# Optimization experiments

Hardware: AMD Instinct MI355X
Metric: run time of the kernel (lower is better)

The kernel has to match this reference:

```python
import jax, jax.numpy as jnp
import numpy as np

CHUNK = 128
KERNEL_EPS = 1e-4
ATTN_EPS = 1e-6


def _gaussian_orthogonal_random_matrix(nb_rows, nb_cols, seed=0):
    # scaling=0: rows of stacked orthogonal blocks, scaled by chi-distributed norms
    rng = np.random.default_rng(seed)
    blocks = []
    n_full = nb_rows // nb_cols
    for _ in range(n_full):
        qm, _ = np.linalg.qr(rng.standard_normal((nb_cols, nb_cols)))
        blocks.append(qm.T)
    rem = nb_rows - n_full * nb_cols
    if rem > 0:
        qm, _ = np.linalg.qr(rng.standard_normal((nb_cols, nb_cols)))
        blocks.append(qm.T[:rem])
    mat = np.concatenate(blocks, axis=0)
    multiplier = np.linalg.norm(rng.standard_normal((nb_rows, nb_cols)), axis=1)
    return (multiplier[:, None] * mat).astype(np.float32)


def softmax_kernel(data, proj, is_query):
    # data: [b,h,n,d], proj: [m,d]
    d = data.shape[-1]
    m = proj.shape[0]
    data_normalizer = d ** -0.25
    ratio = m ** -0.5
    data_dash = jnp.einsum('bhnd,md->bhnm', data * data_normalizer, proj)
    diag_data = (data ** 2).sum(-1, keepdims=True) * 0.5 * (data_normalizer ** 2)
    if is_query:
        stab = jnp.max(data_dash, axis=-1, keepdims=True)
    else:
        stab = jnp.max(data_dash)
    return ratio * (jnp.exp(data_dash - diag_data - stab) + KERNEL_EPS)


def chunked_causal_linear_attention(qf, kf, v):
    # qf,kf: [b,h,n,m]; v: [b,h,n,e]
    b, h, n, m = qf.shape
    e = v.shape[-1]
    nc = n // CHUNK
    to_chunks = lambda t: t.reshape(b, h, nc, CHUNK, -1).transpose(2, 0, 1, 3, 4)
    qc, kc, vc = to_chunks(qf), to_chunks(kf), to_chunks(v)  # [nc,b,h,c,*]

    def step(carry, xs):
        Z, S = carry  # Z: [b,h,m], S: [b,h,m,e]
        q, k, vv = xs
        k_cum = Z[:, :, None, :] + jnp.cumsum(k, axis=2)          # [b,h,c,m]
        D_inv = 1.0 / jnp.einsum('bhcm,bhcm->bhc', q, k_cum + ATTN_EPS)
        ctx = jnp.einsum('bhcm,bhce->bhcme', k, vv)               # [b,h,c,m,e]
        ctx_cum = S[:, :, None, :, :] + jnp.cumsum(ctx, axis=2)
        out = jnp.einsum('bhcme,bhcm,bhc->bhce', ctx_cum, q, D_inv)
        return (k_cum[:, :, -1, :], ctx_cum[:, :, -1, :, :]), out

    Z0 = jnp.zeros((b, h, m), qf.dtype)
    S0 = jnp.zeros((b, h, m, e), qf.dtype)
    (Z, S), outs = jax.lax.scan(jax.checkpoint(step), (Z0, S0), (qc, kc, vc))
    out = outs.transpose(1, 2, 0, 3, 4).reshape(b, h, n, e)
    return out, Z, S


def setup_inputs() -> dict:
    key = jax.random.key(0)
    kq, kk, kv = jax.random.split(key, 3)
    B, H, N, D, M = 2, 8, 4096, 64, 256
    q = jax.random.normal(kq, (B, H, N, D), dtype=jnp.float32)
    k = jax.random.normal(kk, (B, H, N, D), dtype=jnp.float32)
    v = jax.random.normal(kv, (B, H, N, D), dtype=jnp.float32)
    projection_matrix = jnp.asarray(_gaussian_orthogonal_random_matrix(M, D))
    return {"q": q, "k": k, "v": v, "projection_matrix": projection_matrix,
            "inferrring_states": 1}


def reference(q, k, v, projection_matrix, inferrring_states):
    qf = softmax_kernel(q, projection_matrix, is_query=True)
    kf = softmax_kernel(k, projection_matrix, is_query=False)
    out, Z, S = chunked_causal_linear_attention(qf, kf, v)
    return (out, Z, S)
```

## Files before the change

### kernel.cpp

```cpp
#include <hip/hip_runtime.h>

typedef unsigned short ushort_t;
typedef __attribute__((ext_vector_type(8))) short bf16x8;
typedef __attribute__((ext_vector_type(8))) _Float16 f16x8;
typedef __attribute__((ext_vector_type(16))) float f32x16;

#define NORMC 0.35355339059327373f
#define DIAGC 0.0625f
#define RATIO 0.0625f
#define KEPS  1e-4f
#define AEPS  1e-6f
#define KAPPA (RATIO*KEPS)

__device__ __forceinline__ unsigned short f2bf(float f){
  unsigned u = __float_as_uint(f);
  unsigned r = (u + 0x7FFFu + ((u >> 16) & 1u)) >> 16;
  return (unsigned short)r;
}
__device__ __forceinline__ float bf2f(unsigned short h){
  return __uint_as_float(((unsigned)h) << 16);
}
__device__ __forceinline__ unsigned enc_f(float f){
  unsigned u = __float_as_uint(f);
  return (u & 0x80000000u) ? ~u : (u | 0x80000000u);
}
__device__ __forceinline__ float dec_f(unsigned e){
  unsigned b = (e & 0x80000000u) ? (e ^ 0x80000000u) : ~e;
  return __uint_as_float(b);
}
__device__ __forceinline__ unsigned short h2u(_Float16 h){
  union { _Float16 h; unsigned short u; } c; c.h = h; return c.u;
}
__device__ __forceinline__ unsigned pk2h(float a, float b){
  return (unsigned)h2u((_Float16)a) | ((unsigned)h2u((_Float16)b) << 16);
}
__device__ __forceinline__ unsigned cvt2(unsigned wrd, float alpha){
  float lo = bf2f((ushort_t)(wrd & 0xffffu));
  float hi = bf2f((ushort_t)(wrd >> 16));
  return (unsigned)f2bf(fmaf(alpha, lo, KAPPA)) |
         ((unsigned)f2bf(fmaf(alpha, hi, KAPPA)) << 16);
}

__global__ void k_prep(const float* __restrict__ proj, ushort_t* __restrict__ pjh,
                       unsigned* __restrict__ kmax){
  int t = threadIdx.x;
  if (t == 0) *kmax = 0u;
  for (int d = 0; d < 64; ++d){
    float val = NORMC * proj[t*64 + d];
    pjh[t*64 + d] = h2u((_Float16)val);
  }
}

__launch_bounds__(512, 2)
__global__ void k_chunkF(const float* __restrict__ kk, const float* __restrict__ v,
                         const ushort_t* __restrict__ pjh,
                         ushort_t* __restrict__ kfp, float* __restrict__ Zl,
                         float* __restrict__ Sl, float* __restrict__ vsb,
                         unsigned* __restrict__ kmax, float* __restrict__ lmArr)
{
  extern __shared__ char sm[];
  char* Bp = sm;
  char* Xh = sm + 32768;
  char* Xl = sm + 49152;
  char* ob = sm;
  char* kT = sm + 65536;
  char* vT = sm + 131072;
  float* dsm  = (float*)(sm + 147456);
  float* wred = (float*)(sm + 147968);

  int tid = threadIdx.x;
  int w   = tid >> 6;
  int wr  = w & 3;
  int wc  = w >> 2;
  int lane= tid & 63;
  int l31 = lane & 31;
  int half= lane >> 5;
  int cb  = (int)blockIdx.x;
  int bh  = cb >> 5, j = cb & 31;
  int row0 = bh*4096 + j*128;

  for (int i = tid; i < 2048; i += 512){
    int m = i >> 3, c8 = i & 7;
    int rgn = ((m>>5)*4 + (c8>>1))*2 + (c8&1);
    int slot = (m & 31) ^ ((rgn & 7) << 2);
    *(uint4*)(Bp + rgn*512 + slot*16) = *(const uint4*)(pjh + m*64 + c8*8);
  }
  #pragma unroll
  for (int it = 0; it < 4; ++it){
    int g = it*512 + tid;
    int row = g >> 4, c4 = g & 15;
    float4 xv = *(const float4*)(kk + (size_t)(row0+row)*64 + c4*4);
    _Float16 h0=(_Float16)xv.x, h1=(_Float16)xv.y, h2=(_Float16)xv.z, h3=(_Float16)xv.w;
    float l0 = xv.x-(float)h0, l1 = xv.y-(float)h1, l2 = xv.z-(float)h2, l3 = xv.w-(float)h3;
    int rgn = ((row>>5)*4 + (c4>>2))*2 + ((c4>>1)&1);
    int off = rgn*512 + (((row&31) ^ ((c4>>1)<<2)))*16 + (c4&1)*8;
    uint2 ph; ph.x = (unsigned)h2u(h0)|((unsigned)h2u(h1)<<16);
              ph.y = (unsigned)h2u(h2)|((unsigned)h2u(h3)<<16);
    uint2 pl; pl.x = pk2h(l0,l1); pl.y = pk2h(l2,l3);
    *(uint2*)(Xh + off) = ph;
    *(uint2*)(Xl + off) = pl;
    float ssq = xv.x*xv.x + xv.y*xv.y + xv.z*xv.z + xv.w*xv.w;
    ssq += __shfl_xor(ssq, 1); ssq += __shfl_xor(ssq, 2);
    ssq += __shfl_xor(ssq, 4); ssq += __shfl_xor(ssq, 8);
    if ((tid & 15) == 0) dsm[row] = ssq;
  }
  {
    int e = tid & 63, c0 = tid >> 6;
    int swz = (e & 15) << 4;
    #pragma unroll
    for (int u=0; u<16; ++u){
      int c = c0 + u*8;
      *(ushort_t*)(vT + e*256 + ((c*2) ^ swz)) = f2bf(v[(size_t)(row0+c)*64 + e]);
    }
  }
  __syncthreads();

  f16x8 ah[4], al[4];
  #pragma unroll
  for (int ks = 0; ks < 4; ++ks){
    int rgn = (wr*4+ks)*2+half;
    int off = rgn*512 + ((l31 ^ ((2*ks+half)<<2)))*16;
    ah[ks] = *(const f16x8*)(Xh + off);
    al[ks] = *(const f16x8*)(Xl + off);
  }
  f32x16 acc[4];
  #pragma unroll
  for (int ct=0; ct<4; ++ct){
    #pragma unroll
    for (int r=0; r<16; ++r) acc[ct][r] = 0.f;
  }
  #pragma unroll
  for (int ks = 0; ks < 4; ++ks){
    #pragma unroll
    for (int ct=0; ct<4; ++ct){
      int ctg = wc*4 + ct;
      int rgn = (ctg*4+ks)*2+half;
      f16x8 bv = *(const f16x8*)(Bp + rgn*512 + ((l31 ^ ((2*ks+half)<<2)))*16);
      acc[ct] = __builtin_amdgcn_mfma_f32_32x32x16_f16(ah[ks], bv, acc[ct], 0, 0, 0);
      acc[ct] = __builtin_amdgcn_mfma_f32_32x32x16_f16(al[ks], bv, acc[ct], 0, 0, 0);
    }
  }

  {
    float wm = acc[0][0];
    #pragma unroll
    for (int ct=0; ct<4; ++ct){
      #pragma unroll
      for (int r=0; r<16; ++r) wm = fmaxf(wm, acc[ct][r]);
    }
    #pragma unroll
    for (int s=1; s<32; s<<=1) wm = fmaxf(wm, __shfl_xor(wm, s));
    wm = fmaxf(wm, __shfl_xor(wm, 32));
    if (lane == 0) wred[w] = wm;
  }
  __syncthreads();
  float lmb = wred[0];
  #pragma unroll
  for (int i=1;i<8;++i) lmb = fmaxf(lmb, wred[i]);
  if (tid == 0){
    lmArr[cb] = lmb;
    atomicMax(kmax, enc_f(lmb));
  }
  float dgv[16];
  #pragma unroll
  for (int r=0; r<16; ++r)
    dgv[r] = DIAGC * dsm[32*wr + (r&3) + 8*(r>>2) + 4*half];

  #pragma unroll
  for (int ct=0; ct<4; ++ct){
    int m = wc*128 + ct*32 + l31;
    int swm = (m & 15) << 4;
    #pragma unroll
    for (int g=0; g<4; ++g){
      unsigned pk0=0, pk1=0;
      #pragma unroll
      for (int rr=0; rr<4; ++rr){
        int r = g*4 + rr;
        int c = 32*wr + rr + 8*g + 4*half;
        float e = __expf(acc[ct][r] - dgv[r] - lmb);
        unsigned b = f2bf(e);
        if (rr < 2) pk0 |= b << (16*rr); else pk1 |= b << (16*(rr-2));
        *(ushort_t*)(ob + c*512 + ((m*2) ^ ((c&15)<<4))) = (ushort_t)b;
      }
      int c0 = 32*wr + 8*g + 4*half;
      *(uint2*)(kT + m*256 + ((c0*2) ^ swm)) = make_uint2(pk0, pk1);
    }
  }
  __syncthreads();

  f32x16 acc2[2], accz, avs[2];
  #pragma unroll
  for (int et=0;et<2;++et){
    #pragma unroll
    for (int r=0;r<16;++r){ acc2[et][r]=0.f; avs[et][r]=0.f; }
  }
  #pragma unroll
  for (int r=0;r<16;++r) accz[r]=0.f;
  bf16x8 onesB, onesA;
  #pragma unroll
  for (int i=0;i<8;++i){
    onesB[i] = (l31==0) ? (short)0x3F80 : (short)0;
    onesA[i] = (short)0x3F80;
  }
  int mrow = 32*w + l31;
  int swm2 = (mrow & 15) << 4;
  #pragma unroll
  for (int ks=0; ks<8; ++ks){
    int koff = ks*32 + half*16;
    bf16x8 af = *(const bf16x8*)(kT + mrow*256 + (koff ^ swm2));
    bf16x8 b0 = *(const bf16x8*)(vT + (l31)*256      + (koff ^ ((l31&15)<<4)));
    bf16x8 b1 = *(const bf16x8*)(vT + (32+l31)*256   + (koff ^ (((32+l31)&15)<<4)));
    acc2[0] = __builtin_amdgcn_mfma_f32_32x32x16_bf16(af, b0, acc2[0], 0, 0, 0);
    acc2[1] = __builtin_amdgcn_mfma_f32_32x32x16_bf16(af, b1, acc2[1], 0, 0, 0);
    accz    = __builtin_amdgcn_mfma_f32_32x32x16_bf16(af, onesB, accz, 0, 0, 0);
    if (w == 0){
      avs[0] = __builtin_amdgcn_mfma_f32_32x32x16_bf16(onesA, b0, avs[0], 0, 0, 0);
      avs[1] = __builtin_amdgcn_mfma_f32_32x32x16_bf16(onesA, b1, avs[1], 0, 0, 0);
    }
  }
  #pragma unroll
  for (int r=0; r<16; ++r){
    int m = 32*w + (r&3) + 8*(r>>2) + 4*half;
    #pragma unroll
    for (int et=0; et<2; ++et)
      Sl[(size_t)cb*16384 + (size_t)m*64 + et*32 + l31] = acc2[et][r];
  }
  if (l31 == 0){
    #pragma unroll
    for (int r=0; r<16; ++r){
      int m = 32*w + (r&3) + 8*(r>>2) + 4*half;
      Zl[(size_t)cb*256 + m] = accz[r];
    }
  }
  if (w == 0 && half == 0){
    vsb[(size_t)cb*64 + l31]      = avs[0][0];
    vsb[(size_t)cb*64 + 32 + l31] = avs[1][0];
  }
  {
    ushort_t* dst = kfp + (size_t)row0*256;
    for (int i = tid; i < 4096; i += 512){
      int row = i >> 5, s = i & 31;
      uint4 d = *(const uint4*)(ob + row*512 + ((s*16) ^ ((row&15)<<4)));
      *(uint4*)(dst + (size_t)row*256 + ((s ^ (row&15)))*8) = d;
    }
  }
}

__launch_bounds__(256)
__global__ void k_scan(float* __restrict__ Zl, const float* __restrict__ Sl,
                       const float* __restrict__ vsb, const float* __restrict__ lmArr,
                       const unsigned* __restrict__ kmax,
                       ushort_t* __restrict__ S0b,
                       float* __restrict__ outZ, float* __restrict__ outS){
  float gm = dec_f(*kmax);
  int t = threadIdx.x;
  int bh = blockIdx.x / 65;
  int s  = blockIdx.x % 65;
  if (s == 64){
    size_t base = (size_t)(bh*32)*256 + t;
    float rz = 0.f;
    #pragma unroll
    for (int j0=0;j0<32;j0+=8){
      float x[8];
      #pragma unroll
      for (int u=0;u<8;++u){
        int cbx = bh*32 + j0 + u;
        float a = RATIO * __expf(lmArr[cbx] - gm);
        x[u] = fmaf(a, Zl[base + (size_t)(j0+u)*256], KAPPA*128.f);
      }
      #pragma unroll
      for (int u=0;u<8;++u){ Zl[base + (size_t)(j0+u)*256] = rz; rz += x[u]; }
    }
    outZ[(size_t)bh*256 + t] = rz;
  } else {
    int e = t & 63;
    size_t base = (size_t)(bh*32)*16384 + (size_t)s*256 + t;
    float rs = 0.f;
    #pragma unroll
    for (int j0=0;j0<32;j0+=8){
      float x[8];
      #pragma unroll
      for (int u=0;u<8;++u){
        int cbx = bh*32 + j0 + u;
        float a = RATIO * __expf(lmArr[cbx] - gm);
        x[u] = fmaf(a, Sl[base + (size_t)(j0+u)*16384], KAPPA * vsb[(size_t)cbx*64 + e]);
      }
      #pragma unroll
      for (int u=0;u<8;++u){
        S0b[(size_t)(bh*32 + j0+u)*16384 + (size_t)s*256 + t] = f2bf(rs);
        rs += x[u];
      }
    }
    outS[(size_t)bh*16384 + (size_t)s*256 + t] = rs;
  }
}

__launch_bounds__(512, 2)
__global__ void k_outF(const float* __restrict__ q, const ushort_t* __restrict__ pjh,
                       const ushort_t* __restrict__ kfp, const float* __restrict__ v,
                       const ushort_t* __restrict__ S0b, const float* __restrict__ Zp,
                       const float* __restrict__ lmArr, const unsigned* __restrict__ kmax,
                       float* __restrict__ outO)
{
  extern __shared__ char sm[];
  char* Bp  = sm;
  char* Ab  = sm;
  char* qfb = sm + 32768;
  char* Xh  = sm + 32768;
  char* Xl  = sm + 49152;
  char* ktb = sm + 98304;
  char* s0t = sm + 114688;
  char* vTb = sm + 98304;
  float* dsm = (float*)(sm + 122880);
  float* rmx = (float*)(sm + 123392);
  float* qzc = (float*)(sm + 124416);
  float* rsc = (float*)(sm + 125440);
  float* rsf = (float*)(sm + 126464);

  int tid = threadIdx.x;
  int w   = tid >> 6;
  int wr  = w & 3;
  int wc  = w >> 2;
  int lane= tid & 63;
  int l31 = lane & 31;
  int half= lane >> 5;
  int pb  = (int)blockIdx.x;
  int bh  = pb >> 5, j = pb & 31;
  int row0 = bh*4096 + j*128;
  size_t qbase = (size_t)row0*256;

  float gmv = dec_f(*kmax);
  float alpha = RATIO * __expf(lmArr[pb] - gmv);

  for (int i = tid; i < 2048; i += 512){
    int m = i >> 3, c8 = i & 7;
    int rgn = ((m>>5)*4 + (c8>>1))*2 + (c8&1);
    int slot = (m & 31) ^ ((rgn & 7) << 2);
    *(uint4*)(Bp + rgn*512 + slot*16) = *(const uint4*)(pjh + m*64 + c8*8);
  }
  #pragma unroll
  for (int it = 0; it < 4; ++it){
    int g = it*512 + tid;
    int row = g >> 4, c4 = g & 15;
    float4 xv = *(const float4*)(q + (size_t)(row0+row)*64 + c4*4);
    _Float16 h0=(_Float16)xv.x, h1=(_Float16)xv.y, h2=(_Float16)xv.z, h3=(_Float16)xv.w;
    float l0 = xv.x-(float)h0, l1 = xv.y-(float)h1, l2 = xv.z-(float)h2, l3 = xv.w-(float)h3;
    int rgn = ((row>>5)*4 + (c4>>2))*2 + ((c4>>1)&1);
    int off = rgn*512 + (((row&31) ^ ((c4>>1)<<2)))*16 + (c4&1)*8;
    uint2 ph; ph.x = (unsigned)h2u(h0)|((unsigned)h2u(h1)<<16);
              ph.y = (unsigned)h2u(h2)|((unsigned)h2u(h3)<<16);
    uint2 pl; pl.x = pk2h(l0,l1); pl.y = pk2h(l2,l3);
    *(uint2*)(Xh + off) = ph;
    *(uint2*)(Xl + off) = pl;
    float ssq = xv.x*xv.x + xv.y*xv.y + xv.z*xv.z + xv.w*xv.w;
    ssq += __shfl_xor(ssq, 1); ssq += __shfl_xor(ssq, 2);
    ssq += __shfl_xor(ssq, 4); ssq += __shfl_xor(ssq, 8);
    if ((tid & 15) == 0) dsm[row] = ssq;
  }
  __syncthreads();

  f16x8 ah[4], al[4];
  #pragma unroll
  for (int ks = 0; ks < 4; ++ks){
    int rgn = (wr*4+ks)*2+half;
    int off = rgn*512 + ((l31 ^ ((2*ks+half)<<2)))*16;
    ah[ks] = *(const f16x8*)(Xh + off);
    al[ks] = *(const f16x8*)(Xl + off);
  }
  f32x16 acc[4];
  #pragma unroll
  for (int ct=0; ct<4; ++ct){
    #pragma unroll
    for (int r=0; r<16; ++r) acc[ct][r] = 0.f;
  }
  #pragma unroll
  for (int ks = 0; ks < 4; ++ks){
    #pragma unroll
    for (int ct=0; ct<4; ++ct){
      int ctg = wc*4 + ct;
      int rgn = (ctg*4+ks)*2+half;
      f16x8 bv = *(const f16x8*)(Bp + rgn*512 + ((l31 ^ ((2*ks+half)<<2)))*16);
      acc[ct] = __builtin_amdgcn_mfma_f32_32x32x16_f16(ah[ks], bv, acc[ct], 0, 0, 0);
      acc[ct] = __builtin_amdgcn_mfma_f32_32x32x16_f16(al[ks], bv, acc[ct], 0, 0, 0);
    }
  }
  {
    float rmax[16];
    #pragma unroll
    for (int r=0; r<16; ++r){
      float mx = acc[0][r];
      #pragma unroll
      for (int ct=1; ct<4; ++ct) mx = fmaxf(mx, acc[ct][r]);
      #pragma unroll
      for (int s=1; s<32; s<<=1) mx = fmaxf(mx, __shfl_xor(mx, s));
      rmax[r] = mx;
    }
    if (l31 == 0){
      #pragma unroll
      for (int r=0; r<16; ++r)
        rmx[wc*128 + 32*wr + (r&3) + 8*(r>>2) + 4*half] = rmax[r];
    }
  }
  __syncthreads();

  float qzp[16];
  #pragma unroll
  for (int r=0;r<16;++r) qzp[r] = 0.f;
  {
    float dgv[16], stv[16];
    #pragma unroll
    for (int r=0; r<16; ++r){
      int lrow = 32*wr + (r&3) + 8*(r>>2) + 4*half;
      dgv[r] = DIAGC * dsm[lrow];
      stv[r] = fmaxf(rmx[lrow], rmx[128+lrow]);
    }
    #pragma unroll
    for (int ct=0; ct<4; ++ct){
      int m = wc*128 + ct*32 + l31;
      float z0v = Zp[(size_t)pb*256 + m] + AEPS;
      #pragma unroll
      for (int r=0; r<16; ++r){
        int c = 32*wr + (r&3) + 8*(r>>2) + 4*half;
        float e = __expf(acc[ct][r] - dgv[r] - stv[r]);
        unsigned b = f2bf(RATIO*(e + KEPS));
        *(ushort_t*)(qfb + c*512 + ((m*2) ^ ((c&15)<<4))) = (ushort_t)b;
        qzp[r] += bf2f((ushort_t)b) * z0v;
      }
    }
    #pragma unroll
    for (int s=1; s<32; s<<=1){
      #pragma unroll
      for (int r=0;r<16;++r) qzp[r] += __shfl_xor(qzp[r], s);
    }
    if (l31 == 0){
      #pragma unroll
      for (int r=0;r<16;++r)
        qzc[wc*128 + 32*wr + (r&3) + 8*(r>>2) + 4*half] = qzp[r];
    }
  }

  f32x16 accA[2], acc2;
  #pragma unroll
  for (int ct2=0;ct2<2;++ct2){
    #pragma unroll
    for (int r=0;r<16;++r) accA[ct2][r] = 0.f;
  }
  #pragma unroll
  for (int r=0;r<16;++r) acc2[r] = 0.f;

  int arow = 32*wr + l31;
  for (int mt=0; mt<4; ++mt){
    int m0 = mt*64;
    __syncthreads();
    #pragma unroll
    for (int u=0;u<2;++u){
      int ci = tid*2+u; int rr = ci>>3, c8 = ci&7;
      int sw = (c8*16) ^ ((rr&7)<<4);
      uint4 rk = *(const uint4*)(kfp + qbase + (size_t)rr*256 + m0 + c8*8);
      uint4 ck; ck.x = cvt2(rk.x, alpha); ck.y = cvt2(rk.y, alpha);
                ck.z = cvt2(rk.z, alpha); ck.w = cvt2(rk.w, alpha);
      *(uint4*)(ktb + rr*128 + sw) = ck;
    }
    {
      int mm = tid >> 3, c8 = tid & 7;
      uint4 sv = *(const uint4*)(S0b + (size_t)pb*16384 + (size_t)(m0+mm)*64 + c8*8);
      unsigned wds[4] = {sv.x, sv.y, sv.z, sv.w};
      #pragma unroll
      for (int jj=0;jj<4;++jj){
        int e0 = c8*8 + jj*2, e1 = e0 + 1;
        int sw0 = ((e0&7) ^ ((e0>>3)&7)) << 4;
        int sw1 = ((e1&7) ^ ((e1>>3)&7)) << 4;
        *(ushort_t*)(s0t + e0*128 + ((mm*2) ^ sw0)) = (ushort_t)(wds[jj] & 0xffffu);
        *(ushort_t*)(s0t + e1*128 + ((mm*2) ^ sw1)) = (ushort_t)(wds[jj] >> 16);
      }
    }
    __syncthreads();
    #pragma unroll
    for (int ks=0;ks<4;++ks){
      bf16x8 af = *(const bf16x8*)(qfb + arow*512 + ((m0*2 + ks*32 + half*16) ^ ((arow&15)<<4)));
      {
        int er = wc*32 + l31;
        int sw = ((er&7) ^ ((er>>3)&7)) << 4;
        bf16x8 bS = *(const bf16x8*)(s0t + er*128 + ((ks*32 + half*16) ^ sw));
        acc2 = __builtin_amdgcn_mfma_f32_32x32x16_bf16(af, bS, acc2, 0, 0, 0);
      }
      #pragma unroll
      for (int ct2=0;ct2<2;++ct2){
        int c = wc*2 + ct2;
        if (c <= wr){
          int br = c*32 + l31;
          bf16x8 bfv = *(const bf16x8*)(ktb + br*128 + ((ks*32 + half*16) ^ ((br&7)<<4)));
          accA[ct2] = __builtin_amdgcn_mfma_f32_32x32x16_bf16(af, bfv, accA[ct2], 0, 0, 0);
        }
      }
    }
  }

  {
    float p[16];
    #pragma unroll
    for (int r=0;r<16;++r) p[r]=0.f;
    #pragma unroll
    for (int ct2=0;ct2<2;++ct2){
      int c = wc*2 + ct2;
      if (c <= wr){
        #pragma unroll
        for (int r=0;r<16;++r){
          int grow = 32*wr + (r&3) + 8*(r>>2) + 4*half;
          int col  = c*32 + l31;
          float mval = (col <= grow) ? accA[ct2][r] : 0.f;
          p[r] += mval;
          *(ushort_t*)(Ab + grow*256 + ((col*2) ^ ((grow&15)<<4))) = f2bf(mval);
        }
      }
    }
    #pragma unroll
    for (int s=1;s<32;s<<=1){
      #pragma unroll
      for (int r=0;r<16;++r) p[r] += __shfl_xor(p[r], s);
    }
    if (l31 == 0){
      #pragma unroll
      for (int r=0;r<16;++r)
        rsc[wc*128 + 32*wr + (r&3) + 8*(r>>2) + 4*half] = p[r];
    }
  }
  __syncthreads();

  {
    int e = tid & 63, c0 = tid >> 6;
    int swz = (e & 15) << 4;
    #pragma unroll
    for (int u=0; u<16; ++u){
      int c = c0 + u*8;
      *(ushort_t*)(vTb + e*256 + ((c*2) ^ swz)) = f2bf(v[(size_t)(row0+c)*64 + e]);
    }
  }
  __syncthreads();

  #pragma unroll
  for (int ks=0; ks<8; ++ks){
    if (ks <= 2*wr + 1){
      bf16x8 af = *(const bf16x8*)(Ab + arow*256 + ((ks*32 + half*16) ^ ((arow&15)<<4)));
      int er = wc*32 + l31;
      bf16x8 bfv = *(const bf16x8*)(vTb + er*256 + ((ks*32 + half*16) ^ ((er&15)<<4)));
      acc2 = __builtin_amdgcn_mfma_f32_32x32x16_bf16(af, bfv, acc2, 0, 0, 0);
    }
  }
  __syncthreads();
  if (tid < 128)
    rsf[tid] = 1.0f / (rsc[tid] + rsc[128+tid] + qzc[tid] + qzc[128+tid]);
  __syncthreads();
  #pragma unroll
  for (int r=0;r<16;++r){
    int grow = 32*wr + (r&3) + 8*(r>>2) + 4*half;
    int e = wc*32 + l31;
    outO[(size_t)(row0+grow)*64 + e] = acc2[r] * rsf[grow];
  }
}

extern "C" void kernel_launch(void* const* d_in, const int* in_sizes, int n_in,
                              void* d_out, int out_size, void* d_ws, size_t ws_size,
                              hipStream_t stream){
  (void)in_sizes; (void)n_in; (void)out_size; (void)ws_size;
  const float* q    = (const float*)d_in[0];
  const float* k    = (const float*)d_in[1];
  const float* v    = (const float*)d_in[2];
  const float* proj = (const float*)d_in[3];

  char* ws = (char*)d_ws;
  unsigned* kmax = (unsigned*)ws;
  float*    lmA  = (float*)(ws + 256);
  ushort_t* pjh  = (ushort_t*)(ws + 4096);
  ushort_t* kfp  = (ushort_t*)(ws + 65792);
  float*    Zl   = (float*)(ws + 65792 + 33554432);
  float*    Sl   = (float*)(ws + 65792 + 33554432 + 524288);
  ushort_t* S0b  = (ushort_t*)(ws + 65792 + 67633152);
  float*    vsb  = (float*)(ws + 65792 + 67633152 + 16777216);

  float* outO = (float*)d_out;
  float* outZ = outO + (size_t)2*8*4096*64;
  float* outS = outZ + 2*8*256;

  hipFuncSetAttribute((const void*)k_chunkF, hipFuncAttributeMaxDynamicSharedMemorySize, 148480);
  hipFuncSetAttribute((const void*)k_outF,   hipFuncAttributeMaxDynamicSharedMemorySize, 126976);

  k_prep  <<<1,     256, 0, stream>>>(proj, pjh, kmax);
  k_chunkF<<<512,   512, 148480, stream>>>(k, v, pjh, kfp, Zl, Sl, vsb, kmax, lmA);
  k_scan  <<<16*65, 256, 0, stream>>>(Zl, Sl, vsb, lmA, kmax, S0b, outZ, outS);
  k_outF  <<<512,   512, 126976, stream>>>(q, pjh, kfp, v, S0b, Zl, lmA, kmax, outO);
}
```

Measured before the change: 98.24 us.

## Transpose S layout, fold alpha/kappa rescale into MFMA epilogue, shrink outF LDS

The chunk kernel now produces per-chunk S transposed (e-major), so the output kernel can copy S0 and raw kf tiles straight into LDS with 16-byte stores. This removes the scalar scatter and the per-element alpha/kappa conversion. The alpha scaling and the kappa term are applied to the masked intra-chunk scores, and q·Z0 plus the row sums of qf are computed with an extra MFMA against a Z/ones vector. Query features are staged in 64-column slices, which cuts LDS from about 124KB to 75KB and may allow higher occupancy. A small new transpose kernel restores the m-major final S output, at the cost of an extra launch and extra MFMA work.

Result: slower. 147.3 us (+49.9%).

```diff
diff --git a/kernel.cpp b/kernel.cpp
--- a/kernel.cpp
+++ b/kernel.cpp
@@ -33,12 +33,6 @@
 }
 __device__ __forceinline__ unsigned pk2h(float a, float b){
   return (unsigned)h2u((_Float16)a) | ((unsigned)h2u((_Float16)b) << 16);
-}
-__device__ __forceinline__ unsigned cvt2(unsigned wrd, float alpha){
-  float lo = bf2f((ushort_t)(wrd & 0xffffu));
-  float hi = bf2f((ushort_t)(wrd >> 16));
-  return (unsigned)f2bf(fmaf(alpha, lo, KAPPA)) |
-         ((unsigned)f2bf(fmaf(alpha, hi, KAPPA)) << 16);
 }
 
 __global__ void k_prep(const float* __restrict__ proj, ushort_t* __restrict__ pjh,
@@ -188,11 +182,11 @@
   }
   __syncthreads();
 
-  f32x16 acc2[2], accz, avs[2];
+  f32x16 accS[2], accz, avs[2];
   #pragma unroll
   for (int et=0;et<2;++et){
     #pragma unroll
-    for (int r=0;r<16;++r){ acc2[et][r]=0.f; avs[et][r]=0.f; }
+    for (int r=0;r<16;++r){ accS[et][r]=0.f; avs[et][r]=0.f; }
   }
   #pragma unroll
   for (int r=0;r<16;++r) accz[r]=0.f;
@@ -202,28 +196,31 @@
     onesB[i] = (l31==0) ? (short)0x3F80 : (short)0;
     onesA[i] = (short)0x3F80;
   }
+  int erow = (w&1)*32 + l31;
+  int mc0  = ((w>>1)*2 + 0)*32 + l31;
+  int mc1  = ((w>>1)*2 + 1)*32 + l31;
   int mrow = 32*w + l31;
-  int swm2 = (mrow & 15) << 4;
   #pragma unroll
   for (int ks=0; ks<8; ++ks){
     int koff = ks*32 + half*16;
-    bf16x8 af = *(const bf16x8*)(kT + mrow*256 + (koff ^ swm2));
-    bf16x8 b0 = *(const bf16x8*)(vT + (l31)*256      + (koff ^ ((l31&15)<<4)));
-    bf16x8 b1 = *(const bf16x8*)(vT + (32+l31)*256   + (koff ^ (((32+l31)&15)<<4)));
-    acc2[0] = __builtin_amdgcn_mfma_f32_32x32x16_bf16(af, b0, acc2[0], 0, 0, 0);
-    acc2[1] = __builtin_amdgcn_mfma_f32_32x32x16_bf16(af, b1, acc2[1], 0, 0, 0);
-    accz    = __builtin_amdgcn_mfma_f32_32x32x16_bf16(af, onesB, accz, 0, 0, 0);
+    bf16x8 afv = *(const bf16x8*)(vT + erow*256 + (koff ^ ((erow&15)<<4)));
+    bf16x8 bk0 = *(const bf16x8*)(kT + mc0*256 + (koff ^ ((mc0&15)<<4)));
+    bf16x8 bk1 = *(const bf16x8*)(kT + mc1*256 + (koff ^ ((mc1&15)<<4)));
+    bf16x8 afk = *(const bf16x8*)(kT + mrow*256 + (koff ^ ((mrow&15)<<4)));
+    accS[0] = __builtin_amdgcn_mfma_f32_32x32x16_bf16(afv, bk0, accS[0], 0, 0, 0);
+    accS[1] = __builtin_amdgcn_mfma_f32_32x32x16_bf16(afv, bk1, accS[1], 0, 0, 0);
+    accz    = __builtin_amdgcn_mfma_f32_32x32x16_bf16(afk, onesB, accz, 0, 0, 0);
     if (w == 0){
-      avs[0] = __builtin_amdgcn_mfma_f32_32x32x16_bf16(onesA, b0, avs[0], 0, 0, 0);
-      avs[1] = __builtin_amdgcn_mfma_f32_32x32x16_bf16(onesA, b1, avs[1], 0, 0, 0);
+      bf16x8 bv1 = *(const bf16x8*)(vT + (32+l31)*256 + (koff ^ (((32+l31)&15)<<4)));
+      avs[0] = __builtin_amdgcn_mfma_f32_32x32x16_bf16(onesA, afv, avs[0], 0, 0, 0);
+      avs[1] = __builtin_amdgcn_mfma_f32_32x32x16_bf16(onesA, bv1, avs[1], 0, 0, 0);
     }
   }
   #pragma unroll
   for (int r=0; r<16; ++r){
-    int m = 32*w + (r&3) + 8*(r>>2) + 4*half;
-    #pragma unroll
-    for (int et=0; et<2; ++et)
-      Sl[(size_t)cb*16384 + (size_t)m*64 + et*32 + l31] = acc2[et][r];
+    int e = (w&1)*32 + (r&3) + 8*(r>>2) + 4*half;
+    Sl[(size_t)cb*16384 + (size_t)e*256 + ((w>>1)*2+0)*32 + l31] = accS[0][r];
+    Sl[(size_t)cb*16384 + (size_t)e*256 + ((w>>1)*2+1)*32 + l31] = accS[1][r];
   }
   if (l31 == 0){
     #pragma unroll
@@ -251,7 +248,7 @@
                        const float* __restrict__ vsb, const float* __restrict__ lmArr,
                        const unsigned* __restrict__ kmax,
                        ushort_t* __restrict__ S0b,
-                       float* __restrict__ outZ, float* __restrict__ outS){
+                       float* __restrict__ outZ, float* __restrict__ outSt){
   float gm = dec_f(*kmax);
   int t = threadIdx.x;
   int bh = blockIdx.x / 65;
@@ -273,7 +270,6 @@
     }
     outZ[(size_t)bh*256 + t] = rz;
   } else {
-    int e = t & 63;
     size_t base = (size_t)(bh*32)*16384 + (size_t)s*256 + t;
     float rs = 0.f;
     #pragma unroll
@@ -283,7 +279,7 @@
       for (int u=0;u<8;++u){
         int cbx = bh*32 + j0 + u;
         float a = RATIO * __expf(lmArr[cbx] - gm);
-        x[u] = fmaf(a, Sl[base + (size_t)(j0+u)*16384], KAPPA * vsb[(size_t)cbx*64 + e]);
+        x[u] = fmaf(a, Sl[base + (size_t)(j0+u)*16384], KAPPA * vsb[(size_t)cbx*64 + s]);
       }
       #pragma unroll
       for (int u=0;u<8;++u){
@@ -291,7 +287,24 @@
         rs += x[u];
       }
     }
-    outS[(size_t)bh*16384 + (size_t)s*256 + t] = rs;
+    outSt[(size_t)bh*16384 + (size_t)s*256 + t] = rs;
+  }
+}
+
+__launch_bounds__(256)
+__global__ void k_tr(const float* __restrict__ outSt, float* __restrict__ outS){
+  __shared__ float tl[64][65];
+  int tid = threadIdx.x;
+  int bh = blockIdx.x >> 2, mt = blockIdx.x & 3;
+  int m0 = mt*64;
+  for (int i = tid; i < 4096; i += 256){
+    int e = i >> 6, m = i & 63;
+    tl[e][m] = outSt[(size_t)bh*16384 + (size_t)e*256 + m0 + m];
+  }
+  __syncthreads();
+  for (int i = tid; i < 4096; i += 256){
+    int m = i >> 6, e = i & 63;
+    outS[(size_t)bh*16384 + (size_t)(m0+m)*64 + e] = tl[e][m];
   }
 }
 
@@ -303,19 +316,18 @@
                        float* __restrict__ outO)
 {
   extern __shared__ char sm[];
-  char* Bp  = sm;
-  char* Ab  = sm;
-  char* qfb = sm + 32768;
-  char* Xh  = sm + 32768;
-  char* Xl  = sm + 49152;
-  char* ktb = sm + 98304;
-  char* s0t = sm + 114688;
-  char* vTb = sm + 98304;
-  float* dsm = (float*)(sm + 122880);
-  float* rmx = (float*)(sm + 123392);
-  float* qzc = (float*)(sm + 124416);
-  float* rsc = (float*)(sm + 125440);
-  float* rsf = (float*)(sm + 126464);
+  char* Bp   = sm;
+  char* Ab   = sm;
+  char* Xh   = sm + 32768;
+  char* qft  = sm + 32768;
+  char* vTb  = sm + 32768;
+  char* Xl   = sm + 49152;
+  char* ktb  = sm + 49152;
+  char* s0t  = sm + 65536;
+  float* dsm = (float*)(sm + 73728);
+  float* rmx = (float*)(sm + 74240);
+  float* rsc = (float*)(sm + 75264);
+  ushort_t* z0b = (ushort_t*)(sm + 76288);
 
   int tid = threadIdx.x;
   int w   = tid >> 6;
@@ -357,6 +369,7 @@
     ssq += __shfl_xor(ssq, 4); ssq += __shfl_xor(ssq, 8);
     if ((tid & 15) == 0) dsm[row] = ssq;
   }
+  if (tid < 256) z0b[tid] = f2bf(Zp[(size_t)pb*256 + tid] + AEPS);
   __syncthreads();
 
   f16x8 ah[4], al[4];
@@ -403,50 +416,29 @@
   }
   __syncthreads();
 
-  float qzp[16];
-  #pragma unroll
-  for (int r=0;r<16;++r) qzp[r] = 0.f;
-  {
-    float dgv[16], stv[16];
-    #pragma unroll
-    for (int r=0; r<16; ++r){
-      int lrow = 32*wr + (r&3) + 8*(r>>2) + 4*half;
-      dgv[r] = DIAGC * dsm[lrow];
-      stv[r] = fmaxf(rmx[lrow], rmx[128+lrow]);
-    }
-    #pragma unroll
-    for (int ct=0; ct<4; ++ct){
-      int m = wc*128 + ct*32 + l31;
-      float z0v = Zp[(size_t)pb*256 + m] + AEPS;
-      #pragma unroll
-      for (int r=0; r<16; ++r){
-        int c = 32*wr + (r&3) + 8*(r>>2) + 4*half;
-        float e = __expf(acc[ct][r] - dgv[r] - stv[r]);
-        unsigned b = f2bf(RATIO*(e + KEPS));
-        *(ushort_t*)(qfb + c*512 + ((m*2) ^ ((c&15)<<4))) = (ushort_t)b;
-        qzp[r] += bf2f((ushort_t)b) * z0v;
-      }
-    }
-    #pragma unroll
-    for (int s=1; s<32; s<<=1){
-      #pragma unroll
-      for (int r=0;r<16;++r) qzp[r] += __shfl_xor(qzp[r], s);
-    }
-    if (l31 == 0){
-      #pragma unroll
-      for (int r=0;r<16;++r)
-        qzc[wc*128 + 32*wr + (r&3) + 8*(r>>2) + 4*half] = qzp[r];
-    }
-  }
-
-  f32x16 accA[2], acc2;
+  unsigned qpk[2][16];
+  #pragma unroll
+  for (int r=0; r<16; ++r){
+    int lrow = 32*wr + (r&3) + 8*(r>>2) + 4*half;
+    float dg = DIAGC * dsm[lrow];
+    float st = fmaxf(rmx[lrow], rmx[128+lrow]);
+    #pragma unroll
+    for (int p=0; p<2; ++p){
+      float e0 = __expf(acc[2*p][r]   - dg - st);
+      float e1 = __expf(acc[2*p+1][r] - dg - st);
+      qpk[p][r] = (unsigned)f2bf(RATIO*(e0+KEPS)) |
+                  ((unsigned)f2bf(RATIO*(e1+KEPS)) << 16);
+    }
+  }
+
+  f32x16 accA[2], acc2, accQ;
   #pragma unroll
   for (int ct2=0;ct2<2;++ct2){
     #pragma unroll
     for (int r=0;r<16;++r) accA[ct2][r] = 0.f;
   }
   #pragma unroll
-  for (int r=0;r<16;++r) acc2[r] = 0.f;
+  for (int r=0;r<16;++r){ acc2[r] = 0.f; accQ[r] = 0.f; }
 
   int arow = 32*wr + l31;
   for (int mt=0; mt<4; ++mt){
@@ -455,45 +447,60 @@
     #pragma unroll
     for (int u=0;u<2;++u){
       int ci = tid*2+u; int rr = ci>>3, c8 = ci&7;
-      int sw = (c8*16) ^ ((rr&7)<<4);
-      uint4 rk = *(const uint4*)(kfp + qbase + (size_t)rr*256 + m0 + c8*8);
-      uint4 ck; ck.x = cvt2(rk.x, alpha); ck.y = cvt2(rk.y, alpha);
-                ck.z = cvt2(rk.z, alpha); ck.w = cvt2(rk.w, alpha);
-      *(uint4*)(ktb + rr*128 + sw) = ck;
+      *(uint4*)(ktb + rr*128 + ((c8*16) ^ ((rr&7)<<4))) =
+          *(const uint4*)(kfp + qbase + (size_t)rr*256 + m0 + c8*8);
     }
     {
-      int mm = tid >> 3, c8 = tid & 7;
-      uint4 sv = *(const uint4*)(S0b + (size_t)pb*16384 + (size_t)(m0+mm)*64 + c8*8);
-      unsigned wds[4] = {sv.x, sv.y, sv.z, sv.w};
-      #pragma unroll
-      for (int jj=0;jj<4;++jj){
-        int e0 = c8*8 + jj*2, e1 = e0 + 1;
-        int sw0 = ((e0&7) ^ ((e0>>3)&7)) << 4;
-        int sw1 = ((e1&7) ^ ((e1>>3)&7)) << 4;
-        *(ushort_t*)(s0t + e0*128 + ((mm*2) ^ sw0)) = (ushort_t)(wds[jj] & 0xffffu);
-        *(ushort_t*)(s0t + e1*128 + ((mm*2) ^ sw1)) = (ushort_t)(wds[jj] >> 16);
+      int e = tid >> 3, c8 = tid & 7;
+      *(uint4*)(s0t + e*128 + ((c8*16) ^ ((e&7)<<4))) =
+          *(const uint4*)(S0b + (size_t)pb*16384 + (size_t)e*256 + m0 + c8*8);
+    }
+    if (wc == (mt>>1)){
+      int p = mt & 1;
+      #pragma unroll
+      for (int r=0;r<16;++r){
+        int c = 32*wr + (r&3) + 8*(r>>2) + 4*half;
+        int sw = (c&7)<<4;
+        *(ushort_t*)(qft + c*128 + ((l31*2) ^ sw))      = (ushort_t)(qpk[p][r] & 0xffffu);
+        *(ushort_t*)(qft + c*128 + (((32+l31)*2) ^ sw)) = (ushort_t)(qpk[p][r] >> 16);
       }
     }
     __syncthreads();
     #pragma unroll
     for (int ks=0;ks<4;++ks){
-      bf16x8 af = *(const bf16x8*)(qfb + arow*512 + ((m0*2 + ks*32 + half*16) ^ ((arow&15)<<4)));
+      int ko = ks*32 + half*16;
+      bf16x8 af = *(const bf16x8*)(qft + arow*128 + (ko ^ ((arow&7)<<4)));
       {
         int er = wc*32 + l31;
-        int sw = ((er&7) ^ ((er>>3)&7)) << 4;
-        bf16x8 bS = *(const bf16x8*)(s0t + er*128 + ((ks*32 + half*16) ^ sw));
+        bf16x8 bS = *(const bf16x8*)(s0t + er*128 + (ko ^ ((er&7)<<4)));
         acc2 = __builtin_amdgcn_mfma_f32_32x32x16_bf16(af, bS, acc2, 0, 0, 0);
+      }
+      {
+        bf16x8 zb = {};
+        if (l31 == 0) zb = *(const bf16x8*)((const char*)z0b + m0*2 + ko);
+        if (l31 == 1){
+          #pragma unroll
+          for (int i2=0;i2<8;++i2) zb[i2] = (short)0x3F80;
+        }
+        accQ = __builtin_amdgcn_mfma_f32_32x32x16_bf16(af, zb, accQ, 0, 0, 0);
       }
       #pragma unroll
       for (int ct2=0;ct2<2;++ct2){
         int c = wc*2 + ct2;
         if (c <= wr){
           int br = c*32 + l31;
-          bf16x8 bfv = *(const bf16x8*)(ktb + br*128 + ((ks*32 + half*16) ^ ((br&7)<<4)));
-          accA[ct2] = __builtin_amdgcn_mfma_f32_32x32x16_bf16(af, bfv, accA[ct2], 0, 0, 0);
+          bf16x8 bk = *(const bf16x8*)(ktb + br*128 + (ko ^ ((br&7)<<4)));
+          accA[ct2] = __builtin_amdgcn_mfma_f32_32x32x16_bf16(af, bk, accA[ct2], 0, 0, 0);
         }
       }
     }
+  }
+
+  float qzv[16], qfsv[16];
+  #pragma unroll
+  for (int r=0;r<16;++r){
+    qzv[r]  = __shfl(accQ[r], half*32 + 0);
+    qfsv[r] = __shfl(accQ[r], half*32 + 1);
   }
 
   {
@@ -508,16 +515,16 @@
         for (int r=0;r<16;++r){
           int grow = 32*wr + (r&3) + 8*(r>>2) + 4*half;
           int col  = c*32 + l31;
-          float mval = (col <= grow) ? accA[ct2][r] : 0.f;
+          float mval = (col <= grow) ? fmaf(alpha, accA[ct2][r], KAPPA*qfsv[r]) : 0.f;
           p[r] += mval;
           *(ushort_t*)(Ab + grow*256 + ((col*2) ^ ((grow&15)<<4))) = f2bf(mval);
         }
       }
     }
     #pragma unroll
-    for (int s=1;s<32;s<<=1){
-      #pragma unroll
-      for (int r=0;r<16;++r) p[r] += __shfl_xor(p[r], s);
+    for (int s2=1;s2<32;s2<<=1){
+      #pragma unroll
+      for (int r=0;r<16;++r) p[r] += __shfl_xor(p[r], s2);
     }
     if (l31 == 0){
       #pragma unroll
@@ -543,19 +550,16 @@
     if (ks <= 2*wr + 1){
       bf16x8 af = *(const bf16x8*)(Ab + arow*256 + ((ks*32 + half*16) ^ ((arow&15)<<4)));
       int er = wc*32 + l31;
-      bf16x8 bfv = *(const bf16x8*)(vTb + er*256 + ((ks*32 + half*16) ^ ((er&15)<<4)));
-      acc2 = __builtin_amdgcn_mfma_f32_32x32x16_bf16(af, bfv, acc2, 0, 0, 0);
-    }
-  }
-  __syncthreads();
-  if (tid < 128)
-    rsf[tid] = 1.0f / (rsc[tid] + rsc[128+tid] + qzc[tid] + qzc[128+tid]);
-  __syncthreads();
+      bf16x8 bv = *(const bf16x8*)(vTb + er*256 + ((ks*32 + half*16) ^ ((er&15)<<4)));
+      acc2 = __builtin_amdgcn_mfma_f32_32x32x16_bf16(af, bv, acc2, 0, 0, 0);
+    }
+  }
+
   #pragma unroll
   for (int r=0;r<16;++r){
     int grow = 32*wr + (r&3) + 8*(r>>2) + 4*half;
-    int e = wc*32 + l31;
-    outO[(size_t)(row0+grow)*64 + e] = acc2[r] * rsf[grow];
+    float dv = 1.0f / (rsc[grow] + rsc[128+grow] + qzv[r]);
+    outO[(size_t)(row0+grow)*64 + wc*32 + l31] = acc2[r] * dv;
   }
 }
 
@@ -573,20 +577,22 @@
   float*    lmA  = (float*)(ws + 256);
   ushort_t* pjh  = (ushort_t*)(ws + 4096);
   ushort_t* kfp  = (ushort_t*)(ws + 65792);
-  float*    Zl   = (float*)(ws + 65792 + 33554432);
-  float*    Sl   = (float*)(ws + 65792 + 33554432 + 524288);
-  ushort_t* S0b  = (ushort_t*)(ws + 65792 + 67633152);
-  float*    vsb  = (float*)(ws + 65792 + 67633152 + 16777216);
+  float*    Zl   = (float*)(ws + 33620224);
+  float*    Sl   = (float*)(ws + 34144512);
+  ushort_t* S0b  = (ushort_t*)(ws + 67698944);
+  float*    vsb  = (float*)(ws + 84476160);
+  float*    oSt  = (float*)(ws + 84607232);
 
   float* outO = (float*)d_out;
   float* outZ = outO + (size_t)2*8*4096*64;
   float* outS = outZ + 2*8*256;
 
   hipFuncSetAttribute((const void*)k_chunkF, hipFuncAttributeMaxDynamicSharedMemorySize, 148480);
-  hipFuncSetAttribute((const void*)k_outF,   hipFuncAttributeMaxDynamicSharedMemorySize, 126976);
+  hipFuncSetAttribute((const void*)k_outF,   hipFuncAttributeMaxDynamicSharedMemorySize, 76800);
 
   k_prep  <<<1,     256, 0, stream>>>(proj, pjh, kmax);
   k_chunkF<<<512,   512, 148480, stream>>>(k, v, pjh, kfp, Zl, Sl, vsb, kmax, lmA);
-  k_scan  <<<16*65, 256, 0, stream>>>(Zl, Sl, vsb, lmA, kmax, S0b, outZ, outS);
-  k_outF  <<<512,   512, 126976, stream>>>(q, pjh, kfp, v, S0b, Zl, lmA, kmax, outO);
-}
+  k_scan  <<<16*65, 256, 0, stream>>>(Zl, Sl, vsb, lmA, kmax, S0b, outZ, oSt);
+  k_tr    <<<64,    256, 0, stream>>>(oSt, outS);
+  k_outF  <<<512,   512, 76800, stream>>>(q, pjh, kfp, v, S0b, Zl, lmA, kmax, outO);
+}
```
